# Performance work log

Measured on AMD Instinct MI355X. Metric: run time of the kernel, lower is better.

## Reference

```python
import jax, jax.numpy as jnp
import numpy as np

W = 128        # word_size
N_LOC = 16384  # n_locations
B = 64
D_CTRL = 1024
EPS_NORM = 1e-12   # F.normalize eps
EPS_SHARP = 1e-9


def setup_inputs() -> dict:
    key = jax.random.key(0)
    k1, k2, k3, k4, k5 = jax.random.split(key, 5)
    controller_state = jax.random.normal(k1, (B, D_CTRL), dtype=jnp.float32)
    memory = jax.random.uniform(k2, (N_LOC, W), dtype=jnp.float32)
    w_prev = jax.random.uniform(k3, (B, N_LOC), dtype=jnp.float32)
    w_prev = w_prev / jnp.sum(w_prev, axis=-1, keepdims=True)  # valid attention dist
    total_out = 3 * W + 6  # key(W)+beta(1)+gate(1)+shift(3)+gamma(1)+erase(W)+add(W)
    fc_w = jax.random.normal(k4, (total_out, D_CTRL), dtype=jnp.float32) * (1.0 / np.sqrt(D_CTRL))
    fc_b = jax.random.normal(k5, (total_out,), dtype=jnp.float32) * 0.01
    return {"controller_state": controller_state, "memory": memory,
            "w_prev": w_prev, "fc_w": fc_w, "fc_b": fc_b}


def _l2_normalize(x, axis=-1):
    n = jnp.sqrt(jnp.sum(x * x, axis=axis, keepdims=True))
    return x / jnp.maximum(n, EPS_NORM)


def reference(controller_state, memory, w_prev, fc_w, fc_b):
    raw = controller_state @ fc_w.T + fc_b  # [B, 3W+6]
    key = raw[:, :W]
    beta = jax.nn.softplus(raw[:, W:W + 1])
    gate = jax.nn.sigmoid(raw[:, W + 1:W + 2])
    shift = jax.nn.softmax(raw[:, W + 2:W + 5], axis=-1)
    gamma = jax.nn.softplus(raw[:, W + 5:W + 6]) + 1.0
    erase = jax.nn.sigmoid(raw[:, W + 6:2 * W + 6])
    add = jnp.tanh(raw[:, 2 * W + 6:3 * W + 6])

    # content addressing: cosine sim + softmax(beta * sim)
    sim = _l2_normalize(key) @ _l2_normalize(memory).T  # [B, N_LOC]
    w_content = jax.nn.softmax(beta * sim, axis=-1)

    # location addressing
    w_g = gate * w_content + (1.0 - gate) * w_prev
    w_shifted = (shift[:, 0:1] * jnp.roll(w_g, 1, axis=1)
                 + shift[:, 1:2] * w_g
                 + shift[:, 2:3] * jnp.roll(w_g, -1, axis=1))
    w_pow = jnp.clip(w_shifted, EPS_SHARP, None) ** gamma
    w_new = w_pow / (jnp.sum(w_pow, axis=-1, keepdims=True) + EPS_SHARP)

    # write: mean over batch of outer products w_new[b] x erase/add[b]
    # == (w_new^T @ erase) / B  (same math as bmm(...).mean(0), no [B,N,W] temp)
    inv_b = 1.0 / w_new.shape[0]
    erase_mean = jnp.einsum('bn,bw->nw', w_new, erase) * inv_b
    add_mean = jnp.einsum('bn,bw->nw', w_new, add) * inv_b
    new_memory = memory * (1.0 - erase_mean) + add_mean
    return w_new, new_memory
```

## Files before the change

kernel.cpp:

```cpp
#include <hip/hip_runtime.h>
#include <math.h>

#define N_LOC 16384
#define W 128
#define B_SZ 64
#define TOTAL_OUT 390

__device__ __forceinline__ float dot4(float4 a, float4 b) {
    return a.x * b.x + a.y * b.y + a.z * b.z + a.w * b.w;
}
__device__ __forceinline__ float softplus_f(float x) {
    return fmaxf(x, 0.0f) + log1pf(expf(-fabsf(x)));
}
__device__ __forceinline__ float sigmoid_f(float x) {
    return 1.0f / (1.0f + expf(-x));
}
__device__ __forceinline__ float wave_reduce_sum(float v) {
#pragma unroll
    for (int off = 32; off >= 1; off >>= 1) v += __shfl_xor(v, off);
    return v;
}

__global__ __launch_bounds__(256) void kA(const float* __restrict__ cs,
                                          const float* __restrict__ fcw,
                                          const float* __restrict__ fcb,
                                          float* __restrict__ raw) {
    __shared__ float4 cs4[8][256];
    const int t = threadIdx.x;
    const int blk = blockIdx.x;
    const int oc = blk % 26;
    const int btile = blk / 26;

    const float4* csg = reinterpret_cast<const float4*>(cs);
#pragma unroll
    for (int i = 0; i < 8; i++) {
        int f4 = t + 256 * i;
        int row = f4 >> 8;
        int col = f4 & 255;
        cs4[row][col] = csg[(btile * 8 + row) * 256 + col];
    }
    __syncthreads();

    const int lane = t & 63;
    const int wv = t >> 6;
    const float4* fcw4 = reinterpret_cast<const float4*>(fcw);

    for (int ol = wv; ol < 15; ol += 4) {
        const int o = oc * 15 + ol;
        float4 r0 = fcw4[o * 256 + 0 * 64 + lane];
        float4 r1 = fcw4[o * 256 + 1 * 64 + lane];
        float4 r2 = fcw4[o * 256 + 2 * 64 + lane];
        float4 r3 = fcw4[o * 256 + 3 * 64 + lane];
#pragma unroll
        for (int b = 0; b < 8; b++) {
            float acc = dot4(cs4[b][0 * 64 + lane], r0);
            acc += dot4(cs4[b][1 * 64 + lane], r1);
            acc += dot4(cs4[b][2 * 64 + lane], r2);
            acc += dot4(cs4[b][3 * 64 + lane], r3);
            acc = wave_reduce_sum(acc);
            if (lane == 0) {
                raw[(btile * 8 + b) * TOTAL_OUT + o] = acc + fcb[o];
            }
        }
    }
}

__global__ __launch_bounds__(256) void kB(const float* __restrict__ mem,
                                          const float* __restrict__ raw,
                                          float* __restrict__ e_buf,
                                          float* __restrict__ partialS) {
    __shared__ float4 kb4[B_SZ][32];
    __shared__ float betaS[B_SZ];
    const int t = threadIdx.x;
    const int blk = blockIdx.x;

    {
        const int b = t >> 2;
        const int q = t & 3;
        const float* rb = raw + b * TOTAL_OUT;
        const float2* rk = reinterpret_cast<const float2*>(rb) + q * 16;
        float2 v[16];
        float ss = 0.0f;
#pragma unroll
        for (int j = 0; j < 16; j++) {
            v[j] = rk[j];
            ss += v[j].x * v[j].x + v[j].y * v[j].y;
        }
        ss += __shfl_xor(ss, 1);
        ss += __shfl_xor(ss, 2);
        const float beta = softplus_f(rb[W]);
        const float scale = beta / fmaxf(sqrtf(ss), 1e-12f);
        if (q == 0) betaS[b] = beta;
#pragma unroll
        for (int jj = 0; jj < 8; jj++) {
            kb4[b][q * 8 + jj] = make_float4(v[2 * jj].x * scale,
                                             v[2 * jj].y * scale,
                                             v[2 * jj + 1].x * scale,
                                             v[2 * jj + 1].y * scale);
        }
    }
    __syncthreads();

    const int nl = t & 31;
    const int n = blk * 32 + nl;
    const int bg = t >> 5;
    const float4* mrow = reinterpret_cast<const float4*>(mem) + (size_t)n * 32;

    float acc[8];
#pragma unroll
    for (int i = 0; i < 8; i++) acc[i] = 0.0f;
    float nrm = 0.0f;
#pragma unroll 8
    for (int k4 = 0; k4 < 32; k4++) {
        float4 mv = mrow[k4];
        nrm += dot4(mv, mv);
#pragma unroll
        for (int bi = 0; bi < 8; bi++)
            acc[bi] += dot4(kb4[bg * 8 + bi][k4], mv);
    }
    const float r = 1.0f / fmaxf(sqrtf(nrm), 1e-12f);
    float ev[8];
#pragma unroll
    for (int bi = 0; bi < 8; bi++) {
        const int b = bg * 8 + bi;
        float e = __expf(acc[bi] * r - betaS[b]);
        ev[bi] = e;
        e_buf[(size_t)b * N_LOC + n] = e;
    }
#pragma unroll
    for (int bi = 0; bi < 8; bi++) {
        float v = ev[bi];
#pragma unroll
        for (int off = 16; off >= 1; off >>= 1) v += __shfl_xor(v, off);
        ev[bi] = v;
    }
    if (nl == 0) {
#pragma unroll
        for (int bi = 0; bi < 8; bi++)
            partialS[(bg * 8 + bi) * 512 + blk] = ev[bi];
    }
}

__global__ __launch_bounds__(256) void kC(const float* __restrict__ e_buf,
                                          const float* __restrict__ wprev,
                                          const float* __restrict__ raw,
                                          const float* __restrict__ partialS,
                                          float* __restrict__ p_buf,
                                          float* __restrict__ partialP,
                                          float* __restrict__ erase,
                                          float* __restrict__ addv) {
    __shared__ float rC[4];
    __shared__ float cpar[5];
    const int t = threadIdx.x;
    const int blk = blockIdx.x;
    const int b = blk >> 3, c = blk & 7;
    const float* rb = raw + b * TOTAL_OUT;

    const float* ps = partialS + b * 512;
    float sv = ps[t] + ps[t + 256];
    sv = wave_reduce_sum(sv);
    if ((t & 63) == 0) rC[t >> 6] = sv;
    if (t == 0) {
        cpar[0] = sigmoid_f(rb[W + 1]);
        cpar[1] = softplus_f(rb[W + 5]) + 1.0f;
        float s0 = rb[W + 2], s1 = rb[W + 3], s2 = rb[W + 4];
        float m = fmaxf(s0, fmaxf(s1, s2));
        float e0 = expf(s0 - m), e1 = expf(s1 - m), e2 = expf(s2 - m);
        float si = 1.0f / (e0 + e1 + e2);
        cpar[2] = e0 * si;
        cpar[3] = e1 * si;
        cpar[4] = e2 * si;
    }
    __syncthreads();
    const float S = rC[0] + rC[1] + rC[2] + rC[3];

    const float gate = cpar[0];
    const float ga = gate / S;
    const float og = 1.0f - gate;
    const float gm = cpar[1];
    const float sh0 = cpar[2];
    const float sh1 = cpar[3];
    const float sh2 = cpar[4];

    if (c == 0) {
        if (t < 128) erase[b * W + t] = sigmoid_f(rb[W + 6 + t]);
        else         addv[b * W + (t - 128)] = tanhf(rb[2 * W + 6 + (t - 128)]);
    }

    const float* erow = e_buf + (size_t)b * N_LOC;
    const float* wrow = wprev + (size_t)b * N_LOC;
    const int nb = c * 2048 + 8 * t;

    float4 e0v = *reinterpret_cast<const float4*>(erow + nb);
    float4 e1v = *reinterpret_cast<const float4*>(erow + nb + 4);
    float4 w0 = *reinterpret_cast<const float4*>(wrow + nb);
    float4 w1 = *reinterpret_cast<const float4*>(wrow + nb + 4);
    const int nm1 = (nb + N_LOC - 1) & (N_LOC - 1);
    const int np8 = (nb + 8) & (N_LOC - 1);

    float g[10];
    g[0] = ga * erow[nm1] + og * wrow[nm1];
    g[1] = ga * e0v.x + og * w0.x;
    g[2] = ga * e0v.y + og * w0.y;
    g[3] = ga * e0v.z + og * w0.z;
    g[4] = ga * e0v.w + og * w0.w;
    g[5] = ga * e1v.x + og * w1.x;
    g[6] = ga * e1v.y + og * w1.y;
    g[7] = ga * e1v.z + og * w1.z;
    g[8] = ga * e1v.w + og * w1.w;
    g[9] = ga * erow[np8] + og * wrow[np8];

    float p[8];
    float sp = 0.0f;
#pragma unroll
    for (int j = 0; j < 8; j++) {
        float x = fmaxf(sh0 * g[j] + sh1 * g[j + 1] + sh2 * g[j + 2], 1e-9f);
        p[j] = exp2f(gm * __log2f(x));
        sp += p[j];
    }
    *reinterpret_cast<float4*>(p_buf + (size_t)b * N_LOC + nb) =
        make_float4(p[0], p[1], p[2], p[3]);
    *reinterpret_cast<float4*>(p_buf + (size_t)b * N_LOC + nb + 4) =
        make_float4(p[4], p[5], p[6], p[7]);

    sp = wave_reduce_sum(sp);
    __syncthreads();
    if ((t & 63) == 0) rC[t >> 6] = sp;
    __syncthreads();
    if (t == 0) partialP[b * 8 + c] = rC[0] + rC[1] + rC[2] + rC[3];
}

__global__ __launch_bounds__(256) void kD(const float* __restrict__ mem,
                                          const float* __restrict__ erase,
                                          const float* __restrict__ addv,
                                          const float* __restrict__ partialP,
                                          float* __restrict__ p_buf,
                                          float* __restrict__ outmem) {
    __shared__ float invb[B_SZ];
    const int t = threadIdx.x;
    const int blk = blockIdx.x;
    if (t < B_SZ) {
        const float* pp = partialP + t * 8;
        float s = 0.0f;
#pragma unroll
        for (int j = 0; j < 8; j++) s += pp[j];
        invb[t] = 1.0f / (s + 1e-9f);
    }
    __syncthreads();

    const int w = t & 127;
    const int nh = t >> 7;
    const int nb = blk * 32;
    const int nbase = nb + nh * 16;

    float ae[16], aa[16];
#pragma unroll
    for (int i = 0; i < 16; i++) { ae[i] = 0.0f; aa[i] = 0.0f; }

    for (int b = 0; b < B_SZ; b++) {
        const float ib = invb[b] * (1.0f / 64.0f);
        const float wei = erase[b * W + w] * ib;
        const float wai = addv[b * W + w] * ib;
        const float4* pr4 =
            reinterpret_cast<const float4*>(p_buf + (size_t)b * N_LOC + nbase);
#pragma unroll
        for (int i4 = 0; i4 < 4; i4++) {
            float4 v = pr4[i4];
            ae[i4 * 4 + 0] += v.x * wei; aa[i4 * 4 + 0] += v.x * wai;
            ae[i4 * 4 + 1] += v.y * wei; aa[i4 * 4 + 1] += v.y * wai;
            ae[i4 * 4 + 2] += v.z * wei; aa[i4 * 4 + 2] += v.z * wai;
            ae[i4 * 4 + 3] += v.w * wei; aa[i4 * 4 + 3] += v.w * wai;
        }
    }
#pragma unroll
    for (int i = 0; i < 16; i++) {
        const int n = nbase + i;
        float mv = mem[(size_t)n * W + w];
        outmem[(size_t)n * W + w] = mv * (1.0f - ae[i]) + aa[i];
    }
    __syncthreads();
    const int b8 = t >> 5, nl = t & 31;
#pragma unroll
    for (int bi = 0; bi < 8; bi++) {
        const int b = bi * 8 + b8;
        const size_t idx = (size_t)b * N_LOC + nb + nl;
        p_buf[idx] *= invb[b];
    }
}

extern "C" void kernel_launch(void* const* d_in, const int* in_sizes, int n_in,
                              void* d_out, int out_size, void* d_ws, size_t ws_size,
                              hipStream_t stream) {
    const float* cs    = (const float*)d_in[0];
    const float* mem   = (const float*)d_in[1];
    const float* wprev = (const float*)d_in[2];
    const float* fcw   = (const float*)d_in[3];
    const float* fcb   = (const float*)d_in[4];

    float* out = (float*)d_out;
    float* p_buf = out;
    float* emem = out + (size_t)B_SZ * N_LOC;

    float* wsf = (float*)d_ws;
    float* raw      = wsf;
    float* erase    = raw + 24960;
    float* addv     = erase + 8192;
    float* partialS = addv + 8192;
    float* partialP = partialS + 32768;

    kA<<<208, 256, 0, stream>>>(cs, fcw, fcb, raw);
    kB<<<512, 256, 0, stream>>>(mem, raw, emem, partialS);
    kC<<<512, 256, 0, stream>>>(emem, wprev, raw, partialS, p_buf, partialP,
                                erase, addv);
    kD<<<512, 256, 0, stream>>>(mem, erase, addv, partialP, p_buf, emem);
}
```

Baseline: 68.91 us.

## Fuse controller projection into content-scoring kernel, recomputing key rows per block

```diff
diff --git a/kernel.cpp b/kernel.cpp
--- a/kernel.cpp
+++ b/kernel.cpp
@@ -21,89 +21,101 @@
     return v;
 }
 
-__global__ __launch_bounds__(256) void kA(const float* __restrict__ cs,
-                                          const float* __restrict__ fcw,
-                                          const float* __restrict__ fcb,
-                                          float* __restrict__ raw) {
-    __shared__ float4 cs4[8][256];
+__global__ __launch_bounds__(512) void k1_scores(const float* __restrict__ cs,
+                                                 const float* __restrict__ fcw,
+                                                 const float* __restrict__ fcb,
+                                                 const float* __restrict__ mem,
+                                                 float* __restrict__ e_buf,
+                                                 float* __restrict__ partialS,
+                                                 float* __restrict__ rawS,
+                                                 float* __restrict__ erase,
+                                                 float* __restrict__ addv) {
+    __shared__ float4 cs8[8][256];
+    __shared__ float raw8[8][132];
+    __shared__ float4 kb4[8][32];
+    __shared__ float betaS8[8];
+    __shared__ float wls[8][8];
+
     const int t = threadIdx.x;
     const int blk = blockIdx.x;
-    const int oc = blk % 26;
-    const int btile = blk / 26;
+    const int bg = blk >> 5;
+    const int nc = blk & 31;
+    const int lane = t & 63;
+    const int wv = t >> 6;
 
     const float4* csg = reinterpret_cast<const float4*>(cs);
 #pragma unroll
-    for (int i = 0; i < 8; i++) {
-        int f4 = t + 256 * i;
+    for (int i = 0; i < 4; i++) {
+        int f4 = t + 512 * i;
         int row = f4 >> 8;
         int col = f4 & 255;
-        cs4[row][col] = csg[(btile * 8 + row) * 256 + col];
-    }
-    __syncthreads();
-
-    const int lane = t & 63;
-    const int wv = t >> 6;
+        cs8[row][col] = csg[(bg * 8 + row) * 256 + col];
+    }
+    __syncthreads();
+
     const float4* fcw4 = reinterpret_cast<const float4*>(fcw);
-
-    for (int ol = wv; ol < 15; ol += 4) {
-        const int o = oc * 15 + ol;
-        float4 r0 = fcw4[o * 256 + 0 * 64 + lane];
-        float4 r1 = fcw4[o * 256 + 1 * 64 + lane];
-        float4 r2 = fcw4[o * 256 + 2 * 64 + lane];
-        float4 r3 = fcw4[o * 256 + 3 * 64 + lane];
+    for (int ol = wv; ol < 142; ol += 8) {
+        int row, j = 0;
+        if (ol < 134) {
+            row = ol;
+        } else {
+            j = nc * 8 + (ol - 134);
+            row = (j < 128) ? (134 + j) : (262 + (j - 128));
+        }
+        float4 r0 = fcw4[row * 256 + 0 * 64 + lane];
+        float4 r1 = fcw4[row * 256 + 1 * 64 + lane];
+        float4 r2 = fcw4[row * 256 + 2 * 64 + lane];
+        float4 r3 = fcw4[row * 256 + 3 * 64 + lane];
+        const float bias = fcb[row];
 #pragma unroll
         for (int b = 0; b < 8; b++) {
-            float acc = dot4(cs4[b][0 * 64 + lane], r0);
-            acc += dot4(cs4[b][1 * 64 + lane], r1);
-            acc += dot4(cs4[b][2 * 64 + lane], r2);
-            acc += dot4(cs4[b][3 * 64 + lane], r3);
+            float acc = dot4(cs8[b][0 * 64 + lane], r0);
+            acc += dot4(cs8[b][1 * 64 + lane], r1);
+            acc += dot4(cs8[b][2 * 64 + lane], r2);
+            acc += dot4(cs8[b][3 * 64 + lane], r3);
             acc = wave_reduce_sum(acc);
             if (lane == 0) {
-                raw[(btile * 8 + b) * TOTAL_OUT + o] = acc + fcb[o];
+                float val = acc + bias;
+                if (ol < 129) {
+                    raw8[b][ol] = val;
+                } else if (ol < 134) {
+                    rawS[(bg * 8 + b) * 5 + (ol - 129)] = val;
+                } else if (j < 128) {
+                    erase[(bg * 8 + b) * W + j] = sigmoid_f(val);
+                } else {
+                    addv[(bg * 8 + b) * W + (j - 128)] = tanhf(val);
+                }
             }
         }
     }
-}
-
-__global__ __launch_bounds__(256) void kB(const float* __restrict__ mem,
-                                          const float* __restrict__ raw,
-                                          float* __restrict__ e_buf,
-                                          float* __restrict__ partialS) {
-    __shared__ float4 kb4[B_SZ][32];
-    __shared__ float betaS[B_SZ];
-    const int t = threadIdx.x;
-    const int blk = blockIdx.x;
-
-    {
-        const int b = t >> 2;
-        const int q = t & 3;
-        const float* rb = raw + b * TOTAL_OUT;
-        const float2* rk = reinterpret_cast<const float2*>(rb) + q * 16;
-        float2 v[16];
+    __syncthreads();
+
+    if (t < 64) {
+        const int b = t >> 3;
+        const int q = t & 7;
         float ss = 0.0f;
 #pragma unroll
-        for (int j = 0; j < 16; j++) {
-            v[j] = rk[j];
-            ss += v[j].x * v[j].x + v[j].y * v[j].y;
+        for (int jj = 0; jj < 16; jj++) {
+            float v = raw8[b][q * 16 + jj];
+            ss += v * v;
         }
         ss += __shfl_xor(ss, 1);
         ss += __shfl_xor(ss, 2);
-        const float beta = softplus_f(rb[W]);
+        ss += __shfl_xor(ss, 4);
+        const float beta = softplus_f(raw8[b][128]);
         const float scale = beta / fmaxf(sqrtf(ss), 1e-12f);
-        if (q == 0) betaS[b] = beta;
-#pragma unroll
-        for (int jj = 0; jj < 8; jj++) {
-            kb4[b][q * 8 + jj] = make_float4(v[2 * jj].x * scale,
-                                             v[2 * jj].y * scale,
-                                             v[2 * jj + 1].x * scale,
-                                             v[2 * jj + 1].y * scale);
-        }
-    }
-    __syncthreads();
-
-    const int nl = t & 31;
-    const int n = blk * 32 + nl;
-    const int bg = t >> 5;
+        if (q == 0) betaS8[b] = beta;
+#pragma unroll
+        for (int jj = 0; jj < 4; jj++) {
+            kb4[b][q * 4 + jj] = make_float4(raw8[b][q * 16 + 4 * jj + 0] * scale,
+                                             raw8[b][q * 16 + 4 * jj + 1] * scale,
+                                             raw8[b][q * 16 + 4 * jj + 2] * scale,
+                                             raw8[b][q * 16 + 4 * jj + 3] * scale);
+        }
+    }
+    __syncthreads();
+
+    const int n = nc * 512 + t;
     const float4* mrow = reinterpret_cast<const float4*>(mem) + (size_t)n * 32;
 
     float acc[8];
@@ -116,54 +128,47 @@
         nrm += dot4(mv, mv);
 #pragma unroll
         for (int bi = 0; bi < 8; bi++)
-            acc[bi] += dot4(kb4[bg * 8 + bi][k4], mv);
+            acc[bi] += dot4(kb4[bi][k4], mv);
     }
     const float r = 1.0f / fmaxf(sqrtf(nrm), 1e-12f);
     float ev[8];
 #pragma unroll
     for (int bi = 0; bi < 8; bi++) {
-        const int b = bg * 8 + bi;
-        float e = __expf(acc[bi] * r - betaS[b]);
+        float e = __expf(acc[bi] * r - betaS8[bi]);
         ev[bi] = e;
-        e_buf[(size_t)b * N_LOC + n] = e;
+        e_buf[(size_t)(bg * 8 + bi) * N_LOC + n] = e;
     }
 #pragma unroll
     for (int bi = 0; bi < 8; bi++) {
-        float v = ev[bi];
-#pragma unroll
-        for (int off = 16; off >= 1; off >>= 1) v += __shfl_xor(v, off);
-        ev[bi] = v;
-    }
-    if (nl == 0) {
-#pragma unroll
-        for (int bi = 0; bi < 8; bi++)
-            partialS[(bg * 8 + bi) * 512 + blk] = ev[bi];
-    }
-}
-
-__global__ __launch_bounds__(256) void kC(const float* __restrict__ e_buf,
-                                          const float* __restrict__ wprev,
-                                          const float* __restrict__ raw,
-                                          const float* __restrict__ partialS,
-                                          float* __restrict__ p_buf,
-                                          float* __restrict__ partialP,
-                                          float* __restrict__ erase,
-                                          float* __restrict__ addv) {
+        float v = wave_reduce_sum(ev[bi]);
+        if (lane == 0) wls[wv][bi] = v;
+    }
+    __syncthreads();
+    if (t < 8) {
+        float s = 0.0f;
+#pragma unroll
+        for (int w = 0; w < 8; w++) s += wls[w][t];
+        partialS[(bg * 8 + t) * 32 + nc] = s;
+    }
+}
+
+__global__ __launch_bounds__(256) void k2_shift(const float* __restrict__ e_buf,
+                                                const float* __restrict__ wprev,
+                                                const float* __restrict__ rawS,
+                                                const float* __restrict__ partialS,
+                                                float* __restrict__ p_buf,
+                                                float* __restrict__ partialP) {
     __shared__ float rC[4];
     __shared__ float cpar[5];
     const int t = threadIdx.x;
     const int blk = blockIdx.x;
     const int b = blk >> 3, c = blk & 7;
-    const float* rb = raw + b * TOTAL_OUT;
-
-    const float* ps = partialS + b * 512;
-    float sv = ps[t] + ps[t + 256];
-    sv = wave_reduce_sum(sv);
-    if ((t & 63) == 0) rC[t >> 6] = sv;
+
     if (t == 0) {
-        cpar[0] = sigmoid_f(rb[W + 1]);
-        cpar[1] = softplus_f(rb[W + 5]) + 1.0f;
-        float s0 = rb[W + 2], s1 = rb[W + 3], s2 = rb[W + 4];
+        const float* rs = rawS + b * 5;
+        cpar[0] = sigmoid_f(rs[0]);
+        cpar[1] = softplus_f(rs[4]) + 1.0f;
+        float s0 = rs[1], s1 = rs[2], s2 = rs[3];
         float m = fmaxf(s0, fmaxf(s1, s2));
         float e0 = expf(s0 - m), e1 = expf(s1 - m), e2 = expf(s2 - m);
         float si = 1.0f / (e0 + e1 + e2);
@@ -171,8 +176,11 @@
         cpar[3] = e1 * si;
         cpar[4] = e2 * si;
     }
-    __syncthreads();
-    const float S = rC[0] + rC[1] + rC[2] + rC[3];
+    const float* ps = partialS + b * 32;
+    float S = 0.0f;
+#pragma unroll
+    for (int j = 0; j < 32; j++) S += ps[j];
+    __syncthreads();
 
     const float gate = cpar[0];
     const float ga = gate / S;
@@ -181,11 +189,6 @@
     const float sh0 = cpar[2];
     const float sh1 = cpar[3];
     const float sh2 = cpar[4];
-
-    if (c == 0) {
-        if (t < 128) erase[b * W + t] = sigmoid_f(rb[W + 6 + t]);
-        else         addv[b * W + (t - 128)] = tanhf(rb[2 * W + 6 + (t - 128)]);
-    }
 
     const float* erow = e_buf + (size_t)b * N_LOC;
     const float* wrow = wprev + (size_t)b * N_LOC;
@@ -230,12 +233,12 @@
     if (t == 0) partialP[b * 8 + c] = rC[0] + rC[1] + rC[2] + rC[3];
 }
 
-__global__ __launch_bounds__(256) void kD(const float* __restrict__ mem,
-                                          const float* __restrict__ erase,
-                                          const float* __restrict__ addv,
-                                          const float* __restrict__ partialP,
-                                          float* __restrict__ p_buf,
-                                          float* __restrict__ outmem) {
+__global__ __launch_bounds__(256) void k3_update(const float* __restrict__ mem,
+                                                 const float* __restrict__ erase,
+                                                 const float* __restrict__ addv,
+                                                 const float* __restrict__ partialP,
+                                                 float* __restrict__ p_buf,
+                                                 float* __restrict__ outmem) {
     __shared__ float invb[B_SZ];
     const int t = threadIdx.x;
     const int blk = blockIdx.x;
@@ -302,15 +305,15 @@
     float* emem = out + (size_t)B_SZ * N_LOC;
 
     float* wsf = (float*)d_ws;
-    float* raw      = wsf;
-    float* erase    = raw + 24960;
+    float* erase    = wsf;
     float* addv     = erase + 8192;
-    float* partialS = addv + 8192;
-    float* partialP = partialS + 32768;
-
-    kA<<<208, 256, 0, stream>>>(cs, fcw, fcb, raw);
-    kB<<<512, 256, 0, stream>>>(mem, raw, emem, partialS);
-    kC<<<512, 256, 0, stream>>>(emem, wprev, raw, partialS, p_buf, partialP,
-                                erase, addv);
-    kD<<<512, 256, 0, stream>>>(mem, erase, addv, partialP, p_buf, emem);
-}
+    float* rawS     = addv + 8192;
+    float* partialS = rawS + 320;
+    float* partialP = partialS + 2048;
+
+    k1_scores<<<256, 512, 0, stream>>>(cs, fcw, fcb, mem, emem, partialS,
+                                       rawS, erase, addv);
+    k2_shift<<<512, 256, 0, stream>>>(emem, wprev, rawS, partialS,
+                                      p_buf, partialP);
+    k3_update<<<512, 256, 0, stream>>>(mem, erase, addv, partialP, p_buf, emem);
+}
```

Result: slower. 104.1 us (+51.1%).
